# Performance work log

Measured on AMD Instinct MI355X. Metric: run time of the kernel, lower is better.

Reference implementation:

```python
import jax, jax.numpy as jnp
import numpy as np
import math

# --- module config (init_kwargs) ---
DES_R = 2.0
RAD_N, AZI_N, ELE_N = 5, 30, 15
TWO_PI = 2.0 * math.pi
PI = math.pi


def setup_inputs() -> dict:
    key = jax.random.key(0)
    points = jax.random.normal(key, (16, 65536, 3), dtype=jnp.float32)
    return {"points": points}


def _xyz2spherical(pts):
    x, y, z = pts[..., 0], pts[..., 1], pts[..., 2]
    r = jnp.sqrt(x * x + y * y + z * z)
    azi = jnp.arctan2(y, x)
    azi = jnp.where(azi < 0, azi + TWO_PI, azi)  # [0, 2pi)
    ele = jnp.arccos(jnp.clip(z / jnp.maximum(r, 1e-12), -1.0, 1.0))  # [0, pi]
    return r, azi, ele


def _two_nearest(d, step):
    # two smallest distances per point along last axis -> interp weights 1 - d/step
    neg, idx = jax.lax.top_k(-d, 2)
    w = 1.0 + neg / step
    return w, idx


def _voxelize(points):
    B, N, _ = points.shape
    r, azi, ele = _xyz2spherical(points)

    # ---- radial axis: centers at (j+0.5)*step, boundary half-bin clamping ----
    tr = DES_R / RAD_N
    sr = tr / 2
    cr = (jnp.arange(RAD_N, dtype=points.dtype) + 0.5) * tr
    dr = jnp.abs(r[..., None] - cr)  # [B,N,RAD_N]
    low = (r < sr)[..., None]
    dr = jnp.where(low & (dr <= sr), 0.0, dr)               # nearest bin -> weight 1
    dr = jnp.where(low & (dr > tr) & (dr <= tr + sr), tr, dr)  # 2nd bin -> weight 0
    high = ((r > DES_R - sr) & (r <= DES_R))[..., None]
    dr = jnp.where(high & (dr > tr) & (dr <= tr + sr), tr, dr)
    wr, ir = _two_nearest(dr, tr)
    wr = jnp.where((r > DES_R)[..., None], 0.0, wr)  # cull points outside sphere

    # ---- azimuth axis: circular distance (== torch wraparound fixups) ----
    ta = TWO_PI / AZI_N
    ca = (jnp.arange(AZI_N, dtype=points.dtype) + 0.5) * ta
    da = jnp.abs(azi[..., None] - ca)
    da = jnp.minimum(da, TWO_PI - da)
    wa, ia = _two_nearest(da, ta)
    wa = jnp.where((azi > TWO_PI)[..., None], 0.0, wa)

    # ---- elevation axis: boundary half-bin clamping on both ends ----
    te = PI / ELE_N
    se = te / 2
    ce = (jnp.arange(ELE_N, dtype=points.dtype) + 0.5) * te
    de = jnp.abs(ele[..., None] - ce)
    lo = (ele < se)[..., None]
    de = jnp.where(lo & (de <= se), 0.0, de)
    de = jnp.where(lo & (de > te) & (de <= te + se), te, de)
    hi = ((ele > PI - se) & (ele <= PI))[..., None]
    de = jnp.where(hi & (de <= 0.75 * te), 0.0, de)
    de = jnp.where(hi & (de > te) & (de <= te + se), te, de)
    we, ie = _two_nearest(de, te)
    we = jnp.where((ele > PI)[..., None], 0.0, we)

    # ---- trilinear weights for the 8 (r,a,e) neighbor combos; scatter-add ----
    w8 = (wr[:, :, :, None, None] * wa[:, :, None, :, None] * we[:, :, None, None, :]).reshape(B, N, 8)
    f8 = ((ir[:, :, :, None, None] * AZI_N + ia[:, :, None, :, None]) * ELE_N + ie[:, :, None, None, :]).reshape(B, N, 8)
    f8 = f8 + jnp.arange(B, dtype=f8.dtype)[:, None, None] * (RAD_N * AZI_N * ELE_N)
    hist = jax.ops.segment_sum(w8.reshape(-1), f8.reshape(-1), num_segments=B * RAD_N * AZI_N * ELE_N)
    return hist.reshape(B, 1, RAD_N, AZI_N, ELE_N)


def reference(points):
    return _voxelize(points)
```

## Files before the change

kernel.cpp:

```cpp
#include <hip/hip_runtime.h>
#include <math.h>


constexpr int RAD_N = 5, AZI_N = 30, ELE_N = 15;
constexpr int BINS  = RAD_N * AZI_N * ELE_N;
constexpr int BLOCK = 256;
constexpr int PPT   = 4;
constexpr int PPB   = BLOCK * PPT;
constexpr float FX_SCALE   = 2097152.0f;
constexpr float FX_INV     = 1.0f / 2097152.0f;

__device__ __forceinline__ float fast_atan2_02pi(float y, float x) {
    const float PI_F     = 3.14159265358979f;
    const float TWO_PI_F = 6.28318530717959f;
    const float HALF_PI  = 1.57079632679490f;
    float ax = fabsf(x), ay = fabsf(y);
    float mx = fmaxf(ax, ay), mn = fminf(ax, ay);
    float t  = mn * __builtin_amdgcn_rcpf(mx);
    float t2 = t * t;
    float p = -0.01172120f;
    p = __builtin_fmaf(p, t2,  0.05265332f);
    p = __builtin_fmaf(p, t2, -0.11643287f);
    p = __builtin_fmaf(p, t2,  0.19354346f);
    p = __builtin_fmaf(p, t2, -0.33262347f);
    p = __builtin_fmaf(p, t2,  0.99997726f);
    float th = t * p;
    th = (ay > ax) ? (HALF_PI - th) : th;
    th = (x < 0.0f) ? (PI_F - th) : th;
    th = (y < 0.0f) ? (TWO_PI_F - th) : th;
    return th;
}

__device__ __forceinline__ float fast_acos(float x) {
    const float PI_F = 3.14159265358979f;
    float a = fabsf(x);
    float p = -0.0012624911f;
    p = __builtin_fmaf(p, a,  0.0066700901f);
    p = __builtin_fmaf(p, a, -0.0170881256f);
    p = __builtin_fmaf(p, a,  0.0308918810f);
    p = __builtin_fmaf(p, a, -0.0501743046f);
    p = __builtin_fmaf(p, a,  0.0889789874f);
    p = __builtin_fmaf(p, a, -0.2145988016f);
    p = __builtin_fmaf(p, a,  1.5707963050f);
    float s = __builtin_amdgcn_sqrtf(1.0f - a);
    float r = s * p;
    return (x < 0.0f) ? (PI_F - r) : r;
}

__device__ __forceinline__ unsigned to_fx(float w) {
    float v = __builtin_fmaf(w, FX_SCALE, 0.5f);
    return (unsigned)fmaxf(v, 0.0f);
}

__device__ __forceinline__ void process_point(float x, float y, float z,
                                              unsigned* hist) {
    const float TWO_PI_F = (float)(6.283185307179586);
    const float PI_F     = (float)(3.141592653589793);
    const float tr       = (float)(2.0 / 5.0);
    const float sr       = (float)(2.0 / 5.0 / 2.0);
    const float tr_p_sr  = (float)(0.4 + 0.2);
    const float rhi_lo   = (float)(2.0 - 0.2);
    const float DES_R_F  = 2.0f;
    const float ta       = (float)(6.283185307179586 / 30.0);
    const float te       = (float)(3.141592653589793 / 15.0);
    const float se       = (float)(3.141592653589793 / 30.0);
    const float te_p_se  = (float)(3.141592653589793 / 15.0 + 3.141592653589793 / 30.0);
    const float te075    = (float)(0.75 * (3.141592653589793 / 15.0));
    const float pi_m_se  = (float)(3.141592653589793 - 3.141592653589793 / 30.0);
    const float inv_tr   = (float)(5.0 / 2.0);
    const float inv_ta   = (float)(30.0 / 6.283185307179586);
    const float inv_te   = (float)(15.0 / 3.141592653589793);

    float r = __builtin_amdgcn_sqrtf(x * x + y * y + z * z);
    if (r > DES_R_F) return;

    float azi = fast_atan2_02pi(y, x);
    float cz = z * __builtin_amdgcn_rcpf(fmaxf(r, 1e-12f));
    cz = fminf(fmaxf(cz, -1.0f), 1.0f);
    float ele = fast_acos(cz);

    int ra = (int)(r * inv_tr);
    if (ra > RAD_N - 1) ra = RAD_N - 1;
    float cra = ((float)ra + 0.5f) * tr;
    int rb = (r > cra) ? ra + 1 : ra - 1;
    rb = (rb < 0) ? 1 : ((rb > RAD_N - 1) ? RAD_N - 2 : rb);
    float dra = fabsf(r - cra);
    float drb = fabsf(r - ((float)rb + 0.5f) * tr);
    {
        bool lowR  = r < sr;
        bool highR = (r > rhi_lo);
        if (lowR) {
            dra = (dra <= sr) ? 0.0f : ((dra > tr && dra <= tr_p_sr) ? tr : dra);
            drb = (drb <= sr) ? 0.0f : ((drb > tr && drb <= tr_p_sr) ? tr : drb);
        }
        if (highR) {
            if (dra > tr && dra <= tr_p_sr) dra = tr;
            if (drb > tr && drb <= tr_p_sr) drb = tr;
        }
    }
    float wra = 1.0f - dra * inv_tr;
    float wrb = 1.0f - drb * inv_tr;

    int aa = (int)(azi * inv_ta);
    if (aa > AZI_N - 1) aa = AZI_N - 1;
    float caa = ((float)aa + 0.5f) * ta;
    int ab = (azi > caa) ? aa + 1 : aa - 1;
    ab = (ab < 0) ? AZI_N - 1 : ((ab > AZI_N - 1) ? 0 : ab);
    float daa = fabsf(azi - caa);
    daa = fminf(daa, TWO_PI_F - daa);
    float dab = fabsf(azi - ((float)ab + 0.5f) * ta);
    dab = fminf(dab, TWO_PI_F - dab);
    float waa = 1.0f - daa * inv_ta;
    float wab = 1.0f - dab * inv_ta;

    int ea = (int)(ele * inv_te);
    if (ea > ELE_N - 1) ea = ELE_N - 1;
    float cea = ((float)ea + 0.5f) * te;
    int eb = (ele > cea) ? ea + 1 : ea - 1;
    eb = (eb < 0) ? 1 : ((eb > ELE_N - 1) ? ELE_N - 2 : eb);
    float dea = fabsf(ele - cea);
    float deb = fabsf(ele - ((float)eb + 0.5f) * te);
    {
        bool lowE  = ele < se;
        bool highE = (ele > pi_m_se) && (ele <= PI_F);
        if (lowE) {
            dea = (dea <= se) ? 0.0f : ((dea > te && dea <= te_p_se) ? te : dea);
            deb = (deb <= se) ? 0.0f : ((deb > te && deb <= te_p_se) ? te : deb);
        }
        if (highE) {
            dea = (dea <= te075) ? 0.0f : ((dea > te && dea <= te_p_se) ? te : dea);
            deb = (deb <= te075) ? 0.0f : ((deb > te && deb <= te_p_se) ? te : deb);
        }
    }
    float wea = 1.0f - dea * inv_te;
    float web = 1.0f - deb * inv_te;

    int rbase_a = ra * (AZI_N * ELE_N), rbase_b = rb * (AZI_N * ELE_N);
    int abase_a = aa * ELE_N,           abase_b = ab * ELE_N;
    float w_aa = wra * waa, w_ab = wra * wab;
    float w_ba = wrb * waa, w_bb = wrb * wab;

    atomicAdd(&hist[rbase_a + abase_a + ea], to_fx(w_aa * wea));
    atomicAdd(&hist[rbase_a + abase_a + eb], to_fx(w_aa * web));
    atomicAdd(&hist[rbase_a + abase_b + ea], to_fx(w_ab * wea));
    atomicAdd(&hist[rbase_a + abase_b + eb], to_fx(w_ab * web));
    atomicAdd(&hist[rbase_b + abase_a + ea], to_fx(w_ba * wea));
    atomicAdd(&hist[rbase_b + abase_a + eb], to_fx(w_ba * web));
    atomicAdd(&hist[rbase_b + abase_b + ea], to_fx(w_bb * wea));
    atomicAdd(&hist[rbase_b + abase_b + eb], to_fx(w_bb * web));
}

__global__ __launch_bounds__(BLOCK) void voxel_u32(
    const float* __restrict__ pts, unsigned* __restrict__ ws_u,
    int N, int blocksPerBatch)
{
    __shared__ unsigned hist[BINS];
    for (int j = threadIdx.x; j < BINS; j += BLOCK) hist[j] = 0u;
    __syncthreads();

    const int batch = blockIdx.x / blocksPerBatch;
    const int bib   = blockIdx.x % blocksPerBatch;
    const size_t batch_off = (size_t)batch * N;
    const int i0 = bib * PPB + (int)threadIdx.x * PPT;

    if (i0 + PPT <= N) {
        const float4* src = (const float4*)(pts + (batch_off + i0) * 3);
        float4 q0 = src[0];
        float4 q1 = src[1];
        float4 q2 = src[2];
        float X[PPT] = { q0.x, q0.w, q1.z, q2.y };
        float Y[PPT] = { q0.y, q1.x, q1.w, q2.z };
        float Z[PPT] = { q0.z, q1.y, q2.x, q2.w };
#pragma unroll
        for (int k = 0; k < PPT; ++k)
            process_point(X[k], Y[k], Z[k], hist);
    } else {
        for (int k = 0; k < PPT; ++k) {
            int i = i0 + k;
            if (i < N) {
                size_t p = (batch_off + i) * 3;
                process_point(pts[p], pts[p + 1], pts[p + 2], hist);
            }
        }
    }

    __syncthreads();
    unsigned* ob = ws_u + (size_t)batch * BINS;
    for (int j = threadIdx.x; j < BINS; j += BLOCK) {
        unsigned v = hist[j];
        if (v) atomicAdd(&ob[j], v);
    }
}

__global__ __launch_bounds__(BLOCK) void fx_convert(
    const unsigned* __restrict__ ws_u, float* __restrict__ out, int total)
{
    int i = blockIdx.x * BLOCK + (int)threadIdx.x;
    if (i < total) out[i] = (float)ws_u[i] * FX_INV;
}

extern "C" void kernel_launch(void* const* d_in, const int* in_sizes, int n_in,
                              void* d_out, int out_size, void* d_ws, size_t ws_size,
                              hipStream_t stream) {
    const float* pts = (const float*)d_in[0];
    float* out = (float*)d_out;

    const int B = 16;
    int total = in_sizes[0] / 3;
    int N = total / B;
    int blocksPerBatch = (N + PPB - 1) / PPB;
    int grid = B * blocksPerBatch;

    unsigned* ws_u = (unsigned*)d_ws;
    int rtotal = B * BINS;
    hipMemsetAsync(d_ws, 0, (size_t)rtotal * sizeof(unsigned), stream);
    voxel_u32<<<dim3(grid), dim3(BLOCK), 0, stream>>>(pts, ws_u, N, blocksPerBatch);
    fx_convert<<<dim3((rtotal + BLOCK - 1) / BLOCK), dim3(BLOCK), 0, stream>>>(
        ws_u, out, rtotal);
}
```

Before: 71.51 us.

## Fuse fixed-point conversion into voxel kernel via last-block counter; use 512-thread blocks

Removes the separate conversion kernel. Each batch gets a completion counter, and the last block to finish a batch converts that batch's fixed-point histogram into float output. Block size doubles to 512, which halves the number of blocks and so the number of global histogram flushes. The cost is a threadfence and an atomic counter per block, a serial tail in the last block, and fewer blocks in flight, which reduces parallelism.

```diff
diff --git a/kernel.cpp b/kernel.cpp
--- a/kernel.cpp
+++ b/kernel.cpp
@@ -4,11 +4,11 @@
 
 constexpr int RAD_N = 5, AZI_N = 30, ELE_N = 15;
 constexpr int BINS  = RAD_N * AZI_N * ELE_N;
-constexpr int BLOCK = 256;
+constexpr int BLOCK = 512;
 constexpr int PPT   = 4;
 constexpr int PPB   = BLOCK * PPT;
-constexpr float FX_SCALE   = 2097152.0f;
-constexpr float FX_INV     = 1.0f / 2097152.0f;
+constexpr float FX_SCALE = 2097152.0f;
+constexpr float FX_INV   = 1.0f / 2097152.0f;
 
 __device__ __forceinline__ float fast_atan2_02pi(float y, float x) {
     const float PI_F     = 3.14159265358979f;
@@ -150,11 +150,12 @@
     atomicAdd(&hist[rbase_b + abase_b + eb], to_fx(w_bb * web));
 }
 
-__global__ __launch_bounds__(BLOCK) void voxel_u32(
+__global__ __launch_bounds__(BLOCK) void voxel_fused(
     const float* __restrict__ pts, unsigned* __restrict__ ws_u,
-    int N, int blocksPerBatch)
+    float* __restrict__ out, int N, int blocksPerBatch)
 {
     __shared__ unsigned hist[BINS];
+    __shared__ int isLast;
     for (int j = threadIdx.x; j < BINS; j += BLOCK) hist[j] = 0u;
     __syncthreads();
 
@@ -190,13 +191,23 @@
         unsigned v = hist[j];
         if (v) atomicAdd(&ob[j], v);
     }
-}
-
-__global__ __launch_bounds__(BLOCK) void fx_convert(
-    const unsigned* __restrict__ ws_u, float* __restrict__ out, int total)
-{
-    int i = blockIdx.x * BLOCK + (int)threadIdx.x;
-    if (i < total) out[i] = (float)ws_u[i] * FX_INV;
+
+    __threadfence();
+    if (threadIdx.x == 0) {
+        unsigned* ctr = ws_u + (size_t)16 * BINS + batch;
+        unsigned prev = __hip_atomic_fetch_add(ctr, 1u, __ATOMIC_ACQ_REL,
+                                               __HIP_MEMORY_SCOPE_AGENT);
+        isLast = (prev == (unsigned)(blocksPerBatch - 1));
+    }
+    __syncthreads();
+    if (isLast) {
+        float* od = out + (size_t)batch * BINS;
+        for (int j = threadIdx.x; j < BINS; j += BLOCK) {
+            unsigned v = __hip_atomic_load(&ob[j], __ATOMIC_RELAXED,
+                                           __HIP_MEMORY_SCOPE_AGENT);
+            od[j] = (float)v * FX_INV;
+        }
+    }
 }
 
 extern "C" void kernel_launch(void* const* d_in, const int* in_sizes, int n_in,
@@ -212,9 +223,7 @@
     int grid = B * blocksPerBatch;
 
     unsigned* ws_u = (unsigned*)d_ws;
-    int rtotal = B * BINS;
-    hipMemsetAsync(d_ws, 0, (size_t)rtotal * sizeof(unsigned), stream);
-    voxel_u32<<<dim3(grid), dim3(BLOCK), 0, stream>>>(pts, ws_u, N, blocksPerBatch);
-    fx_convert<<<dim3((rtotal + BLOCK - 1) / BLOCK), dim3(BLOCK), 0, stream>>>(
-        ws_u, out, rtotal);
-}
+    size_t zero_bytes = ((size_t)B * BINS + B) * sizeof(unsigned);
+    hipMemsetAsync(d_ws, 0, zero_bytes, stream);
+    voxel_fused<<<dim3(grid), dim3(BLOCK), 0, stream>>>(pts, ws_u, out, N, blocksPerBatch);
+}
```

Result: slower. 129.1 us (+80.6%).
